# Kernel tuning notes

Hardware: AMD Instinct MI355X
Metric: run time of the kernel (lower is better)

The kernel has to match this reference:

```python
import jax, jax.numpy as jnp
import numpy as np

ALPHA = 4.0  # spikingjelly default Sigmoid surrogate alpha
BN_EPS = 1e-5

@jax.custom_vjp
def spike(x):
    return (x >= 0.0).astype(x.dtype)

def _spike_fwd(x):
    return spike(x), x

def _spike_bwd(res, g):
    s = jax.nn.sigmoid(ALPHA * res)
    return (g * ALPHA * s * (1.0 - s),)

spike.defvjp(_spike_fwd, _spike_bwd)

def lif(x, tau=2.0, vth=1.0):
    # MultiStepLIFNode: hard reset (v_reset=0), detach_reset=True, scan over time axis 0
    def step(v, xt):
        h = v + (xt - v) / tau          # charge
        s = spike(h - vth)              # fire (surrogate grad)
        v_next = h * (1.0 - jax.lax.stop_gradient(s))  # detached hard reset to 0
        return v_next, s
    _, out = jax.lax.scan(step, jnp.zeros_like(x[0]), x)
    return out

def conv_bn(x, w, b, g, be, m, var):
    # x: [TB, C, N]; 1x1 Conv1d is a channel GEMM, then eval-mode BatchNorm1d
    y = jnp.einsum('oc,bcn->bon', w, x) + b[None, :, None]
    inv = g / jnp.sqrt(var + BN_EPS)
    return (y - m[None, :, None]) * inv[None, :, None] + be[None, :, None]

def setup_inputs() -> dict:
    key = jax.random.key(0)
    T, B, C, H, W = 4, 32, 512, 14, 14
    ks = jax.random.split(key, 32)
    d = {'x': jax.random.normal(ks[0], (T, B, C, H, W), dtype=jnp.float32)}
    scale = 1.0 / np.sqrt(C)
    i = 1
    for p in ['q', 'k', 'v', 'p']:
        d[p + '_cw'] = jax.random.normal(ks[i], (C, C), dtype=jnp.float32) * scale; i += 1
        d[p + '_cb'] = jax.random.normal(ks[i], (C,), dtype=jnp.float32) * 0.1; i += 1
        d[p + '_bg'] = jnp.ones((C,), dtype=jnp.float32)
        d[p + '_bb'] = jnp.zeros((C,), dtype=jnp.float32)
        d[p + '_bm'] = jax.random.normal(ks[i], (C,), dtype=jnp.float32) * 0.1; i += 1
        d[p + '_bv'] = jax.random.uniform(ks[i], (C,), dtype=jnp.float32, minval=0.5, maxval=1.5); i += 1
    d['push_w'] = jnp.asarray(1.0, dtype=jnp.float32)
    d['pull_w'] = jnp.asarray(1.0, dtype=jnp.float32)
    d['pp_bias'] = jnp.asarray(0.0, dtype=jnp.float32)
    return d

def reference(x,
              q_cw, q_cb, q_bg, q_bb, q_bm, q_bv,
              k_cw, k_cb, k_bg, k_bb, k_bm, k_bv,
              v_cw, v_cb, v_bg, v_bb, v_bm, v_bv,
              p_cw, p_cb, p_bg, p_bb, p_bm, p_bv,
              push_w, pull_w, pp_bias):
    T, B, C, H, W = x.shape
    N = H * W
    nh = 8
    hd = C // nh
    scale = 0.125

    xs = lif(x)                                   # head_lif, [T,B,C,H,W]
    xf = xs.reshape(T * B, C, N)
    q = conv_bn(xf, q_cw, q_cb, q_bg, q_bb, q_bm, q_bv).reshape(T, B, C, N)
    k = conv_bn(xf, k_cw, k_cb, k_bg, k_bb, k_bm, k_bv).reshape(T, B, C, N)
    v = conv_bn(xf, v_cw, v_cb, v_bg, v_bb, v_bm, v_bv).reshape(T, B, C, N)

    q_on = lif(q)
    q_off = lif(-q)

    def to_heads(t):  # [T,B,C,N] -> [T,B,nh,N,hd]
        return jnp.swapaxes(t, -1, -2).reshape(T, B, N, nh, hd).transpose(0, 1, 3, 2, 4)

    q_on_h = to_heads(q_on)
    q_off_h = to_heads(q_off)
    k_h = to_heads(lif(k))
    v_h = to_heads(lif(v))

    pw = jax.nn.softplus(push_w)
    pl = jax.nn.softplus(pull_w)
    diff = pw * q_on_h - pl * q_off_h + pp_bias   # push-pull gating
    q_pp = lif(diff)

    kv = jnp.einsum('tbhnd,tbhne->tbhde', k_h, v_h)      # k^T @ v, [T,B,h,hd,hd]
    o = jnp.einsum('tbhnd,tbhde->tbhne', q_pp, kv) * scale

    o = o.transpose(0, 1, 2, 4, 3).reshape(T, B, C, N)   # transpose(3,4) then merge heads
    o = lif(o, vth=0.5)                                   # attn_lif
    o = conv_bn(o.reshape(T * B, C, N), p_cw, p_cb, p_bg, p_bb, p_bm, p_bv)
    return o.reshape(T, B, C, H, W)
```

## Files before the change

### kernel.cpp

```cpp
#include <hip/hip_runtime.h>
#include <hip/hip_bf16.h>
#include <math.h>

typedef unsigned short u16;
typedef unsigned int   u32;

#define CC 512
#define NN 196
#define TT 4
#define BB 32
#define TBB 128
#define NHH 8
#define HD 64

#define ROWS_T  6272
#define CSTRIDE ((size_t)ROWS_T * CC)

typedef __attribute__((ext_vector_type(8))) _Float16 f16x8;
typedef __attribute__((ext_vector_type(4))) float f32x4;

#define ONE_H 0x3C00

__device__ __forceinline__ u16 h_bits(_Float16 h) { return *(u16*)&h; }
__device__ __forceinline__ float h2f(u16 u) { return (float)(*(const _Float16*)&u); }
__device__ __forceinline__ u32 pk2(u16 a, u16 b) { return (u32)a | ((u32)b << 16); }

__device__ __forceinline__ void gld16(const void* g, void* l) {
    __builtin_amdgcn_global_load_lds(
        (const __attribute__((address_space(1))) void*)g,
        (__attribute__((address_space(3))) void*)l, 16, 0, 0);
}

__global__ __launch_bounds__(256) void k_prep_head(
    const float* __restrict__ x, u16* __restrict__ XS,
    const float* __restrict__ qw, const float* __restrict__ kw,
    const float* __restrict__ vw, const float* __restrict__ pw,
    const float* __restrict__ cb0, const float* __restrict__ bg0, const float* __restrict__ bb0,
    const float* __restrict__ bm0, const float* __restrict__ bv0,
    const float* __restrict__ cb1, const float* __restrict__ bg1, const float* __restrict__ bb1,
    const float* __restrict__ bm1, const float* __restrict__ bv1,
    const float* __restrict__ cb2, const float* __restrict__ bg2, const float* __restrict__ bb2,
    const float* __restrict__ bm2, const float* __restrict__ bv2,
    const float* __restrict__ cb3, const float* __restrict__ bg3, const float* __restrict__ bb3,
    const float* __restrict__ bm3, const float* __restrict__ bv3,
    u16* __restrict__ W2, float* __restrict__ SS, float* __restrict__ SH) {
    __shared__ float T[64][65];
    const int tid = threadIdx.x;

    if (blockIdx.x < 4096) {
        size_t idx = (size_t)blockIdx.x * 256 + tid;
        int g = (int)(idx >> 18);
        size_t rem = idx & 262143;
        const float* Ws = (g == 0) ? qw : (g == 1) ? kw : (g == 2) ? vw : pw;
        float w  = Ws[rem];
        _Float16 h0 = (fabsf(w) < 6.2e-5f) ? (_Float16)0.0f : (_Float16)w;
        float r = (w - (float)h0) * 2048.0f;
        _Float16 h1 = (_Float16)r;
        size_t base = (size_t)g * 524288 + rem;
        W2[base] = h_bits(h0); W2[base + 262144] = h_bits(h1);
        return;
    }
    if (blockIdx.x < 4104) {
        int idx = (blockIdx.x - 4096) * 256 + tid;
        int g = idx >> 9, o = idx & 511;
        const float* cb = g == 0 ? cb0 : g == 1 ? cb1 : g == 2 ? cb2 : cb3;
        const float* bg = g == 0 ? bg0 : g == 1 ? bg1 : g == 2 ? bg2 : bg3;
        const float* bb = g == 0 ? bb0 : g == 1 ? bb1 : g == 2 ? bb2 : bb3;
        const float* bm = g == 0 ? bm0 : g == 1 ? bm1 : g == 2 ? bm2 : bm3;
        const float* bv = g == 0 ? bv0 : g == 1 ? bv1 : g == 2 ? bv2 : bv3;
        float inv = bg[o] / sqrtf(bv[o] + 1e-5f);
        SS[g * 512 + o] = inv;
        SH[g * 512 + o] = (cb[o] - bm[o]) * inv + bb[o];
        return;
    }

    const int hidx = blockIdx.x - 4104;
    const int n0 = (hidx & 3) * 64;
    const int b  = (hidx >> 2) & 31;
    const int c_base = (hidx >> 7) * 64;
    const int c_l = tid >> 4;
    const int n4  = (tid & 15) * 4;
    const bool lv = (n0 + n4) < NN;
    const int n_r = tid >> 2;
    const int cq  = (tid & 3) * 16;
    const bool wv = (n0 + n_r) < NN;

    float v[4][4];
    #pragma unroll
    for (int k = 0; k < 4; ++k)
        #pragma unroll
        for (int j = 0; j < 4; ++j) v[k][j] = 0.f;

    for (int t = 0; t < TT; ++t) {
        const size_t xb = ((size_t)(t * BB + b) * CC + c_base) * NN;
        float s[4][4];
        #pragma unroll
        for (int k = 0; k < 4; ++k) {
            const int c = c_l + 16 * k;
            float4 xv = make_float4(0.f, 0.f, 0.f, 0.f);
            if (lv) xv = *(const float4*)(x + xb + (size_t)c * NN + n0 + n4);
            float xa[4] = {xv.x, xv.y, xv.z, xv.w};
            #pragma unroll
            for (int j = 0; j < 4; ++j) {
                float h = v[k][j] + (xa[j] - v[k][j]) * 0.5f;
                s[k][j] = (h >= 1.f) ? 1.f : 0.f;
                v[k][j] = (h >= 1.f) ? 0.f : h;
            }
        }
        __syncthreads();
        #pragma unroll
        for (int k = 0; k < 4; ++k)
            #pragma unroll
            for (int j = 0; j < 4; ++j) T[c_l + 16 * k][n4 + j] = s[k][j];
        __syncthreads();
        if (wv) {
            const size_t ob = ((size_t)(t * BB + b) * NN + n0 + n_r) * CC + c_base + cq;
            u16 u[16];
            #pragma unroll
            for (int m = 0; m < 16; ++m) u[m] = (T[cq + m][n_r] != 0.f) ? ONE_H : 0;
            uint4 q0 = make_uint4(pk2(u[0],u[1]),  pk2(u[2],u[3]),  pk2(u[4],u[5]),  pk2(u[6],u[7]));
            uint4 q1 = make_uint4(pk2(u[8],u[9]),  pk2(u[10],u[11]),pk2(u[12],u[13]),pk2(u[14],u[15]));
            *(uint4*)(XS + ob)     = q0;
            *(uint4*)(XS + ob + 8) = q1;
        }
        __syncthreads();
    }
}

__global__ __launch_bounds__(256) void k_gemm_qkv(const u16* __restrict__ S, const u16* __restrict__ W2,
                                                  const float* __restrict__ scale, const float* __restrict__ shift,
                                                  u16* __restrict__ QS, u16* __restrict__ KS, u16* __restrict__ VS,
                                                  const float* __restrict__ PW, const float* __restrict__ PL,
                                                  const float* __restrict__ PB) {
    __shared__ __align__(16) u16 smem[24576];
    u16* Xt  = smem;
    u16* WtF = smem + 8192;
    const int tid  = threadIdx.x;
    const int lane = tid & 63;
    const int w    = tid >> 6;
    const int bid  = blockIdx.x;
    const int work = (bid & 7) * 294 + (bid >> 3);
    const int rrt  = work / 12;
    const int gw   = work - rrt * 12;
    const int g    = gw >> 2;
    const int wtile = gw & 3;
    const int rr0  = rrt * 32;
    const u16* Wb = W2 + (size_t)g * 524288 + (size_t)(wtile * 128) * CC;
    const float* scl = scale + g * 512;
    const float* shf = shift + g * 512;

    const int lrow8  = lane >> 3;
    const int gchunk = ((lane & 7) ^ lrow8) * 8;
    const int l15 = lane & 15;
    const int q4  = lane >> 4;
    const int wm = (w >> 1) * 64, wn = (w & 1) * 64;

    const size_t arow0 = (size_t)w * CSTRIDE + (size_t)rr0 * CC;

    f32x4 acc[4][4];
    f32x4 zz = {0.f, 0.f, 0.f, 0.f};
    #pragma unroll
    for (int i = 0; i < 4; ++i)
        #pragma unroll
        for (int j = 0; j < 4; ++j) acc[i][j] = zz;

    for (int c0 = 0; c0 < CC; c0 += 64) {
        __syncthreads();
        #pragma unroll
        for (int i = 0; i < 4; ++i) {
            int p = w * 4 + i;
            gld16(S + arow0 + (size_t)(i * 8 + lrow8) * CC + c0 + gchunk, &Xt[p * 512]);
        }
        #pragma unroll
        for (int i = 0; i < 8; ++i) {
            int lin = w * 8 + i;
            int s = lin >> 4, p = lin & 15;
            gld16(Wb + (size_t)s * 262144 + (size_t)(p * 8 + lrow8) * CC + c0 + gchunk,
                  WtF + s * 8192 + p * 512);
        }
        __syncthreads();

        #pragma unroll
        for (int ks = 0; ks < 2; ++ks) {
            const int cpo = ((ks * 4 + q4) ^ (l15 & 7)) * 8;
            f16x8 sf[4], sflo[4];
            #pragma unroll
            for (int i = 0; i < 4; ++i) {
                sf[i]   = *(const f16x8*)&Xt[(wm + i * 16 + l15) * 64 + cpo];
                sflo[i] = sf[i] * (_Float16)0.00048828125f;
            }
            #pragma unroll
            for (int s = 0; s < 2; ++s) {
                f16x8 wf[4];
                #pragma unroll
                for (int i = 0; i < 4; ++i)
                    wf[i] = *(const f16x8*)&WtF[s * 8192 + (wn + i * 16 + l15) * 64 + cpo];
                #pragma unroll
                for (int mt = 0; mt < 4; ++mt)
                    #pragma unroll
                    for (int nt = 0; nt < 4; ++nt)
                        acc[mt][nt] = __builtin_amdgcn_mfma_f32_16x16x32_f16(
                            s ? sflo[mt] : sf[mt], wf[nt], acc[mt][nt], 0, 0, 0);
            }
        }
    }

    const float pwv = (g == 0) ? log1pf(expf(PW[0])) : 0.f;
    const float plv = (g == 0) ? log1pf(expf(PL[0])) : 0.f;
    const float pbv = (g == 0) ? PB[0] : 0.f;
    u16* OUT = (g == 0) ? QS : (g == 1) ? KS : VS;
    float* LY = (float*)smem;
    const int pairid = w & 1;
    const int pr  = tid >> 7;
    const int idx = tid & 127;

    #pragma unroll
    for (int cc = 0; cc < 2; ++cc) {
        __syncthreads();
        #pragma unroll
        for (int ntl = 0; ntl < 2; ++ntl) {
            const int nt = cc * 2 + ntl;
            const int o  = wtile * 128 + wn + nt * 16 + l15;
            const float sc = scl[o], sh = shf[o];
            const int col32 = ntl * 16 + l15;
            #pragma unroll
            for (int mt = 0; mt < 4; ++mt) {
                const int tr0 = wm + mt * 16 + q4 * 4;
                #pragma unroll
                for (int r = 0; r < 4; ++r)
                    LY[(pairid * 128 + tr0 + r) * 33 + col32] = acc[mt][nt][r] * sc + sh;
            }
        }
        __syncthreads();
        #pragma unroll
        for (int stp = 0; stp < 4; ++stp) {
            const int chain = stp * 128 + idx;
            const int nn  = chain >> 4;
            const int c2  = (chain & 15) * 2;
            const int rr  = rr0 + nn;
            const float* Lp = &LY[(pr * 128 + nn) * 33 + c2];
            float ya[4][2];
            #pragma unroll
            for (int t = 0; t < 4; ++t) {
                ya[t][0] = Lp[t * 32 * 33];
                ya[t][1] = Lp[t * 32 * 33 + 1];
            }
            const int ocol = wtile * 128 + pr * 64 + cc * 32 + c2;
            u32* op = (u32*)(OUT + (size_t)rr * CC + ocol);
            if (g == 0) {
                float von[2] = {0.f, 0.f}, voff[2] = {0.f, 0.f}, vpp[2] = {0.f, 0.f};
                #pragma unroll
                for (int t = 0; t < 4; ++t) {
                    u16 sp2[2];
                    #pragma unroll
                    for (int j = 0; j < 2; ++j) {
                        float qv = ya[t][j], h;
                        h = von[j]  + ( qv - von[j] ) * 0.5f; bool s1 = (h >= 1.f); von[j]  = s1 ? 0.f : h;
                        h = voff[j] + (-qv - voff[j]) * 0.5f; bool s2 = (h >= 1.f); voff[j] = s2 ? 0.f : h;
                        float diff = pwv * (s1 ? 1.f : 0.f) - plv * (s2 ? 1.f : 0.f) + pbv;
                        h = vpp[j] + (diff - vpp[j]) * 0.5f; bool sp = (h >= 1.f); vpp[j] = sp ? 0.f : h;
                        sp2[j] = sp ? ONE_H : 0;
                    }
                    op[t * (CSTRIDE / 2)] = pk2(sp2[0], sp2[1]);
                }
            } else {
                float vm[2] = {0.f, 0.f};
                #pragma unroll
                for (int t = 0; t < 4; ++t) {
                    u16 s2[2];
                    #pragma unroll
                    for (int j = 0; j < 2; ++j) {
                        float h = vm[j] + (ya[t][j] - vm[j]) * 0.5f;
                        bool s = (h >= 1.f); vm[j] = s ? 0.f : h;
                        s2[j] = s ? ONE_H : 0;
                    }
                    op[t * (CSTRIDE / 2)] = pk2(s2[0], s2[1]);
                }
            }
        }
    }
}

__global__ __launch_bounds__(256) void k_attn(const u16* __restrict__ Q, const u16* __restrict__ K,
                                              const u16* __restrict__ V, u16* __restrict__ OS) {
    __shared__ __align__(16) u16 sm[19584];
    u16* Kt  = sm;
    u16* Vt  = sm + 8192;
    u16* Qs  = sm;
    u16* kvT = sm + 14976;

    const int tid = threadIdx.x;
    const int tb  = blockIdx.x >> 3;
    const int h   = blockIdx.x & 7;
    const size_t gb = (size_t)tb * NN * CC + (size_t)h * HD;

    const int srow = tid >> 2;
    const int sdq  = (tid & 3) * 16;

    const int lane = tid & 63;
    const int w    = tid >> 6;
    const int l15  = lane & 15;
    const int kb8  = (lane >> 4) * 8;
    const int quad = (lane >> 4) * 4;
    const int dh = (w >> 1) * 32, eh = (w & 1) * 32;

    f32x4 accA[2][2];
    f32x4 zz = {0.f, 0.f, 0.f, 0.f};
    #pragma unroll
    for (int i = 0; i < 2; ++i)
        #pragma unroll
        for (int j = 0; j < 2; ++j) accA[i][j] = zz;

    const uint4 z4 = make_uint4(0, 0, 0, 0);

    #pragma unroll
    for (int ch = 0; ch < 2; ++ch) {
        if (ch) __syncthreads();
        #pragma unroll
        for (int c = 0; c < 2; ++c) {
            int n  = ch * 128 + c * 64 + srow;
            int nl = c * 64 + srow;
            const int nch = nl >> 3, noff = nl & 7;
            bool valid = n < NN;
            const u16* kr = K + gb + (size_t)n * CC + sdq;
            const u16* vr = V + gb + (size_t)n * CC + sdq;
            uint4 ka  = valid ? *(const uint4*)kr : z4;
            uint4 kb2 = valid ? *(const uint4*)(kr + 8) : z4;
            uint4 va  = valid ? *(const uint4*)vr : z4;
            uint4 vb2 = valid ? *(const uint4*)(vr + 8) : z4;
            u32 kwv[8] = {ka.x, ka.y, ka.z, ka.w, kb2.x, kb2.y, kb2.z, kb2.w};
            u32 vwv[8] = {va.x, va.y, va.z, va.w, vb2.x, vb2.y, vb2.z, vb2.w};
            #pragma unroll
            for (int i = 0; i < 8; ++i) {
                const int row0 = sdq + 2 * i;
                const int x0 = (row0 ^ (row0 >> 3)) & 7;
                const int cb0 = ((nch ^ x0) << 3) + noff;
                const int cb1 = ((nch ^ x0 ^ 1) << 3) + noff;
                Kt[row0 * 128 + cb0]       = (u16)(kwv[i] & 0xFFFF);
                Kt[(row0 + 1) * 128 + cb1] = (u16)(kwv[i] >> 16);
                Vt[row0 * 128 + cb0]       = (u16)(vwv[i] & 0xFFFF);
                Vt[(row0 + 1) * 128 + cb1] = (u16)(vwv[i] >> 16);
            }
        }
        __syncthreads();
        #pragma unroll
        for (int k0 = 0; k0 < 128; k0 += 32) {
            f16x8 af[2], bv[2];
            #pragma unroll
            for (int i = 0; i < 2; ++i) {
                const int rowa = dh + i * 16 + l15;
                const int xa = (rowa ^ (rowa >> 3)) & 7;
                const int rowb = eh + i * 16 + l15;
                const int xb = (rowb ^ (rowb >> 3)) & 7;
                const int chnk = (k0 + kb8) >> 3;
                af[i] = *(const f16x8*)&Kt[rowa * 128 + ((chnk ^ xa) << 3)];
                bv[i] = *(const f16x8*)&Vt[rowb * 128 + ((chnk ^ xb) << 3)];
            }
            #pragma unroll
            for (int i = 0; i < 2; ++i)
                #pragma unroll
                for (int j = 0; j < 2; ++j)
                    accA[i][j] = __builtin_amdgcn_mfma_f32_16x16x32_f16(af[i], bv[j], accA[i][j], 0, 0, 0);
        }
    }
    __syncthreads();

    #pragma unroll
    for (int i = 0; i < 2; ++i)
        #pragma unroll
        for (int j = 0; j < 2; ++j) {
            const int e  = eh + j * 16 + l15;
            const int d0 = dh + i * 16 + quad;
            _Float16 h0 = (_Float16)accA[i][j][0];
            _Float16 h1 = (_Float16)accA[i][j][1];
            _Float16 h2 = (_Float16)accA[i][j][2];
            _Float16 h3 = (_Float16)accA[i][j][3];
            uint2 wv = make_uint2(pk2(h_bits(h0), h_bits(h1)), pk2(h_bits(h2), h_bits(h3)));
            *(uint2*)&kvT[e * 72 + d0] = wv;
        }
    #pragma unroll
    for (int p = 0; p < 4; ++p) {
        int n = p * 64 + srow;
        if (n < 208) {
            uint2* qp = (uint2*)&Qs[n * 72 + sdq];
            if (n < NN) {
                const u16* qr = Q + gb + (size_t)n * CC + sdq;
                uint4 qa  = *(const uint4*)qr;
                uint4 qb2 = *(const uint4*)(qr + 8);
                qp[0] = make_uint2(qa.x, qa.y);
                qp[1] = make_uint2(qa.z, qa.w);
                qp[2] = make_uint2(qb2.x, qb2.y);
                qp[3] = make_uint2(qb2.z, qb2.w);
            } else {
                uint2 z2 = make_uint2(0, 0);
                qp[0] = z2; qp[1] = z2; qp[2] = z2; qp[3] = z2;
            }
        }
    }
    __syncthreads();

    f16x8 bq0 = *(const f16x8*)&kvT[(w * 16 + l15) * 72 + 0  + kb8];
    f16x8 bq1 = *(const f16x8*)&kvT[(w * 16 + l15) * 72 + 32 + kb8];
    u16* ob = OS + (size_t)tb * NN * CC + (size_t)h * HD + w * 16 + l15;
    #pragma unroll
    for (int nt = 0; nt < 13; ++nt) {
        f32x4 acc = zz;
        f16x8 a0 = *(const f16x8*)&Qs[(nt * 16 + l15) * 72 + 0  + kb8];
        f16x8 a1 = *(const f16x8*)&Qs[(nt * 16 + l15) * 72 + 32 + kb8];
        acc = __builtin_amdgcn_mfma_f32_16x16x32_f16(a0, bq0, acc, 0, 0, 0);
        acc = __builtin_amdgcn_mfma_f32_16x16x32_f16(a1, bq1, acc, 0, 0, 0);
        #pragma unroll
        for (int r = 0; r < 4; ++r) {
            int n = nt * 16 + quad + r;
            if (n < NN) {
                _Float16 ov = (_Float16)(acc[r] * 0.125f);
                ob[(size_t)n * CC] = h_bits(ov);
            }
        }
    }
}

__global__ __launch_bounds__(256) void k_attn_lif(uint4* __restrict__ OS) {
    const size_t idx = (size_t)blockIdx.x * 256 + threadIdx.x;
    float v[8];
    #pragma unroll
    for (int j = 0; j < 8; ++j) v[j] = 0.f;
    #pragma unroll
    for (int t = 0; t < TT; ++t) {
        const size_t o8 = idx + (size_t)t * (CSTRIDE / 8);
        uint4 d = OS[o8];
        u32 dw[4] = {d.x, d.y, d.z, d.w};
        u16 u[8];
        #pragma unroll
        for (int p = 0; p < 4; ++p) {
            #pragma unroll
            for (int hf = 0; hf < 2; ++hf) {
                int j = p * 2 + hf;
                u16 raw = hf ? (u16)(dw[p] >> 16) : (u16)(dw[p] & 0xFFFF);
                float xv = h2f(raw);
                float h = v[j] + (xv - v[j]) * 0.5f;
                bool s = (h >= 0.5f);
                v[j] = s ? 0.f : h;
                u[j] = s ? ONE_H : 0;
            }
        }
        OS[o8] = make_uint4(pk2(u[0],u[1]), pk2(u[2],u[3]), pk2(u[4],u[5]), pk2(u[6],u[7]));
    }
}

__global__ __launch_bounds__(256) void k_gemm_proj(const u16* __restrict__ S, const u16* __restrict__ W2,
                                                   const float* __restrict__ scale, const float* __restrict__ shift,
                                                   float* __restrict__ Y) {
    __shared__ __align__(16) u16 Xt[128 * 64];
    __shared__ __align__(16) u16 Wt[2][128 * 64];
    const int tid  = threadIdx.x;
    const int lane = tid & 63;
    const int w    = tid >> 6;
    const int bid  = blockIdx.x;
    const int work = (bid & 7) * 98 + (bid >> 3);
    const int ntile = work >> 2;
    const int wtile = work & 3;
    const u16* Sb = S + (size_t)ntile * 128 * CC;
    const u16* Wb = W2 + (size_t)(wtile * 128) * CC;

    const int lrow8  = lane >> 3;
    const int gchunk = ((lane & 7) ^ lrow8) * 8;
    const int l15 = lane & 15;
    const int q4  = lane >> 4;
    const int wm = (w >> 1) * 64, wn = (w & 1) * 64;

    const int tb0 = (ntile * 128) / NN;
    const int bnd = (tb0 + 1) * NN;

    f32x4 acc[4][4];
    f32x4 zz = {0.f, 0.f, 0.f, 0.f};
    #pragma unroll
    for (int i = 0; i < 4; ++i)
        #pragma unroll
        for (int j = 0; j < 4; ++j) acc[i][j] = zz;

    for (int c0 = 0; c0 < CC; c0 += 64) {
        __syncthreads();
        #pragma unroll
        for (int i = 0; i < 4; ++i) {
            int p = w * 4 + i;
            gld16(Sb + (size_t)(p * 8 + lrow8) * CC + c0 + gchunk, &Xt[p * 512]);
        }
        #pragma unroll
        for (int i = 0; i < 8; ++i) {
            int lin = w * 8 + i;
            int s = lin >> 4, p = lin & 15;
            gld16(Wb + (size_t)s * 262144 + (size_t)(p * 8 + lrow8) * CC + c0 + gchunk,
                  &Wt[s][p * 512]);
        }
        __syncthreads();

        #pragma unroll
        for (int ks = 0; ks < 2; ++ks) {
            const int cpo = ((ks * 4 + q4) ^ (l15 & 7)) * 8;
            f16x8 sf[4], sflo[4];
            #pragma unroll
            for (int i = 0; i < 4; ++i) {
                sf[i]   = *(const f16x8*)&Xt[(wn + i * 16 + l15) * 64 + cpo];
                sflo[i] = sf[i] * (_Float16)0.00048828125f;
            }
            #pragma unroll
            for (int s = 0; s < 2; ++s) {
                f16x8 wf[4];
                #pragma unroll
                for (int i = 0; i < 4; ++i)
                    wf[i] = *(const f16x8*)&Wt[s][(wm + i * 16 + l15) * 64 + cpo];
                #pragma unroll
                for (int mt = 0; mt < 4; ++mt)
                    #pragma unroll
                    for (int nt = 0; nt < 4; ++nt)
                        acc[mt][nt] = __builtin_amdgcn_mfma_f32_16x16x32_f16(
                            wf[mt], s ? sflo[nt] : sf[nt], acc[mt][nt], 0, 0, 0);
            }
        }
    }

    #pragma unroll
    for (int mt = 0; mt < 4; ++mt) {
        int o0 = wtile * 128 + wm + mt * 16 + (lane >> 4) * 4;
        #pragma unroll
        for (int nt = 0; nt < 4; ++nt) {
            int row = ntile * 128 + wn + nt * 16 + l15;
            int tb = (row >= bnd) ? tb0 + 1 : tb0;
            int n  = row - tb * NN;
            #pragma unroll
            for (int r = 0; r < 4; ++r)
                Y[((size_t)tb * CC + o0 + r) * NN + n] = acc[mt][nt][r] * scale[o0 + r] + shift[o0 + r];
        }
    }
}

extern "C" void kernel_launch(void* const* d_in, const int* in_sizes, int n_in,
                              void* d_out, int out_size, void* d_ws, size_t ws_size,
                              hipStream_t stream) {
    const float* x    = (const float*)d_in[0];
    const float* q_cw = (const float*)d_in[1];
    const float* q_cb = (const float*)d_in[2];
    const float* q_bg = (const float*)d_in[3];
    const float* q_bb = (const float*)d_in[4];
    const float* q_bm = (const float*)d_in[5];
    const float* q_bv = (const float*)d_in[6];
    const float* k_cw = (const float*)d_in[7];
    const float* k_cb = (const float*)d_in[8];
    const float* k_bg = (const float*)d_in[9];
    const float* k_bb = (const float*)d_in[10];
    const float* k_bm = (const float*)d_in[11];
    const float* k_bv = (const float*)d_in[12];
    const float* v_cw = (const float*)d_in[13];
    const float* v_cb = (const float*)d_in[14];
    const float* v_bg = (const float*)d_in[15];
    const float* v_bb = (const float*)d_in[16];
    const float* v_bm = (const float*)d_in[17];
    const float* v_bv = (const float*)d_in[18];
    const float* p_cw = (const float*)d_in[19];
    const float* p_cb = (const float*)d_in[20];
    const float* p_bg = (const float*)d_in[21];
    const float* p_bb = (const float*)d_in[22];
    const float* p_bm = (const float*)d_in[23];
    const float* p_bv = (const float*)d_in[24];
    const float* pshw = (const float*)d_in[25];
    const float* pllw = (const float*)d_in[26];
    const float* ppb  = (const float*)d_in[27];
    float* out = (float*)d_out;

    if (ws_size < (size_t)242 * 1024 * 1024) return;
    char* W = (char*)d_ws;
    u16*   XS = (u16*)W;
    u16*   QS = (u16*)(W + ((size_t)27 << 20));
    u16*   OS = (u16*)(W + ((size_t)78 << 20));
    u16*   KS = (u16*)(W + ((size_t)182 << 20));
    u16*   VS = (u16*)(W + ((size_t)208 << 20));
    u16*   W2 = (u16*)(W + ((size_t)234 << 20));
    float* SS = (float*)(W + ((size_t)238 << 20));
    float* SH = SS + 2048;

    k_prep_head<<<5128, 256, 0, stream>>>(x, XS,
                                          q_cw, k_cw, v_cw, p_cw,
                                          q_cb, q_bg, q_bb, q_bm, q_bv,
                                          k_cb, k_bg, k_bb, k_bm, k_bv,
                                          v_cb, v_bg, v_bb, v_bm, v_bv,
                                          p_cb, p_bg, p_bb, p_bm, p_bv, W2, SS, SH);

    k_gemm_qkv<<<2352, 256, 0, stream>>>(XS, W2, SS, SH, QS, KS, VS, pshw, pllw, ppb);

    k_attn<<<TBB * NHH, 256, 0, stream>>>(QS, KS, VS, OS);
    k_attn_lif<<<1568, 256, 0, stream>>>((uint4*)OS);

    k_gemm_proj<<<784, 256, 0, stream>>>(OS, W2 + 3 * 524288, SS + 1536, SH + 1536, out);
}
```

Measured before the change: 328.9 us.

## Store K/V spikes channel-major padded so attention loads them via direct-to-LDS copies

The QKV GEMM epilogue now writes K and V spikes transposed into a [T*B, C, 256] layout with zero-padded token tails, instead of token-major rows. The attention kernel then fills its LDS K/V tiles with global_load_lds 16-byte copies using a simple XOR swizzle, replacing the per-element scatter transpose. The prep kernel is split so the pad-zeroing runs separately from the head LIF kernel. The cost is scattered 2-byte global stores in the GEMM epilogue and an extra kernel launch.

```diff
diff --git a/kernel.cpp b/kernel.cpp
--- a/kernel.cpp
+++ b/kernel.cpp
@@ -31,8 +31,7 @@
         (__attribute__((address_space(3))) void*)l, 16, 0, 0);
 }
 
-__global__ __launch_bounds__(256) void k_prep_head(
-    const float* __restrict__ x, u16* __restrict__ XS,
+__global__ __launch_bounds__(256) void k_prep(
     const float* __restrict__ qw, const float* __restrict__ kw,
     const float* __restrict__ vw, const float* __restrict__ pw,
     const float* __restrict__ cb0, const float* __restrict__ bg0, const float* __restrict__ bb0,
@@ -43,12 +42,10 @@
     const float* __restrict__ bm2, const float* __restrict__ bv2,
     const float* __restrict__ cb3, const float* __restrict__ bg3, const float* __restrict__ bb3,
     const float* __restrict__ bm3, const float* __restrict__ bv3,
-    u16* __restrict__ W2, float* __restrict__ SS, float* __restrict__ SH) {
-    __shared__ float T[64][65];
-    const int tid = threadIdx.x;
-
+    u16* __restrict__ W2, float* __restrict__ SS, float* __restrict__ SH,
+    u32* __restrict__ KT32, u32* __restrict__ VT32) {
     if (blockIdx.x < 4096) {
-        size_t idx = (size_t)blockIdx.x * 256 + tid;
+        size_t idx = (size_t)blockIdx.x * 256 + threadIdx.x;
         int g = (int)(idx >> 18);
         size_t rem = idx & 262143;
         const float* Ws = (g == 0) ? qw : (g == 1) ? kw : (g == 2) ? vw : pw;
@@ -61,7 +58,7 @@
         return;
     }
     if (blockIdx.x < 4104) {
-        int idx = (blockIdx.x - 4096) * 256 + tid;
+        int idx = (blockIdx.x - 4096) * 256 + threadIdx.x;
         int g = idx >> 9, o = idx & 511;
         const float* cb = g == 0 ? cb0 : g == 1 ? cb1 : g == 2 ? cb2 : cb3;
         const float* bg = g == 0 ? bg0 : g == 1 ? bg1 : g == 2 ? bg2 : bg3;
@@ -73,11 +70,20 @@
         SH[g * 512 + o] = (cb[o] - bm[o]) * inv + bb[o];
         return;
     }
-
-    const int hidx = blockIdx.x - 4104;
-    const int n0 = (hidx & 3) * 64;
-    const int b  = (hidx >> 2) & 31;
-    const int c_base = (hidx >> 7) * 64;
+    int idx = (blockIdx.x - 4104) * 256 + threadIdx.x;
+    u32* A = (idx >> 16) ? VT32 : KT32;
+    int row = idx & 65535;
+    u32* p = A + (size_t)row * 128 + 98;
+    #pragma unroll
+    for (int k = 0; k < 30; ++k) p[k] = 0;
+}
+
+__global__ __launch_bounds__(256) void k_head_lif(const float* __restrict__ x, u16* __restrict__ XS) {
+    __shared__ float T[64][65];
+    const int tid = threadIdx.x;
+    const int n0 = blockIdx.x * 64;
+    const int b  = blockIdx.y;
+    const int c_base = blockIdx.z * 64;
     const int c_l = tid >> 4;
     const int n4  = (tid & 15) * 4;
     const bool lv = (n0 + n4) < NN;
@@ -129,7 +135,7 @@
 
 __global__ __launch_bounds__(256) void k_gemm_qkv(const u16* __restrict__ S, const u16* __restrict__ W2,
                                                   const float* __restrict__ scale, const float* __restrict__ shift,
-                                                  u16* __restrict__ QS, u16* __restrict__ KS, u16* __restrict__ VS,
+                                                  u16* __restrict__ QS, u16* __restrict__ KT, u16* __restrict__ VT,
                                                   const float* __restrict__ PW, const float* __restrict__ PL,
                                                   const float* __restrict__ PB) {
     __shared__ __align__(16) u16 smem[24576];
@@ -208,7 +214,6 @@
     const float pwv = (g == 0) ? log1pf(expf(PW[0])) : 0.f;
     const float plv = (g == 0) ? log1pf(expf(PL[0])) : 0.f;
     const float pbv = (g == 0) ? PB[0] : 0.f;
-    u16* OUT = (g == 0) ? QS : (g == 1) ? KS : VS;
     float* LY = (float*)smem;
     const int pairid = w & 1;
     const int pr  = tid >> 7;
@@ -232,29 +237,25 @@
             }
         }
         __syncthreads();
-        #pragma unroll
-        for (int stp = 0; stp < 4; ++stp) {
-            const int chain = stp * 128 + idx;
-            const int nn  = chain >> 4;
-            const int c2  = (chain & 15) * 2;
-            const int rr  = rr0 + nn;
-            const float* Lp = &LY[(pr * 128 + nn) * 33 + c2];
-            float ya[4][2];
-            #pragma unroll
-            for (int t = 0; t < 4; ++t) {
-                ya[t][0] = Lp[t * 32 * 33];
-                ya[t][1] = Lp[t * 32 * 33 + 1];
-            }
-            const int ocol = wtile * 128 + pr * 64 + cc * 32 + c2;
-            u32* op = (u32*)(OUT + (size_t)rr * CC + ocol);
-            if (g == 0) {
+        if (g == 0) {
+            #pragma unroll
+            for (int stp = 0; stp < 4; ++stp) {
+                const int chain = stp * 128 + idx;
+                const int nn  = chain >> 4;
+                const int c2  = (chain & 15) * 2;
+                const int rr  = rr0 + nn;
+                const float* Lp = &LY[(pr * 128 + nn) * 33 + c2];
+                const int ocol = wtile * 128 + pr * 64 + cc * 32 + c2;
+                u32* op = (u32*)(QS + (size_t)rr * CC + ocol);
                 float von[2] = {0.f, 0.f}, voff[2] = {0.f, 0.f}, vpp[2] = {0.f, 0.f};
                 #pragma unroll
                 for (int t = 0; t < 4; ++t) {
+                    float ya0 = Lp[t * 32 * 33], ya1 = Lp[t * 32 * 33 + 1];
+                    float yy[2] = {ya0, ya1};
                     u16 sp2[2];
                     #pragma unroll
                     for (int j = 0; j < 2; ++j) {
-                        float qv = ya[t][j], h;
+                        float qv = yy[j], h;
                         h = von[j]  + ( qv - von[j] ) * 0.5f; bool s1 = (h >= 1.f); von[j]  = s1 ? 0.f : h;
                         h = voff[j] + (-qv - voff[j]) * 0.5f; bool s2 = (h >= 1.f); voff[j] = s2 ? 0.f : h;
                         float diff = pwv * (s1 ? 1.f : 0.f) - plv * (s2 ? 1.f : 0.f) + pbv;
@@ -263,26 +264,41 @@
                     }
                     op[t * (CSTRIDE / 2)] = pk2(sp2[0], sp2[1]);
                 }
-            } else {
+            }
+        } else {
+            u16* OUTT = (g == 1) ? KT : VT;
+            #pragma unroll
+            for (int stp = 0; stp < 4; ++stp) {
+                const int chain = stp * 128 + idx;
+                const int nn = chain & 31;
+                const int c2 = (chain >> 5) * 2;
+                const int rr = rr0 + nn;
+                const int b  = rr / 196;
+                const int n  = rr - b * 196;
+                const float* Lp = &LY[(pr * 128 + nn) * 33 + c2];
+                const int c = wtile * 128 + pr * 64 + cc * 32 + c2;
                 float vm[2] = {0.f, 0.f};
                 #pragma unroll
                 for (int t = 0; t < 4; ++t) {
+                    float yy[2] = {Lp[t * 32 * 33], Lp[t * 32 * 33 + 1]};
                     u16 s2[2];
                     #pragma unroll
                     for (int j = 0; j < 2; ++j) {
-                        float h = vm[j] + (ya[t][j] - vm[j]) * 0.5f;
+                        float h = vm[j] + (yy[j] - vm[j]) * 0.5f;
                         bool s = (h >= 1.f); vm[j] = s ? 0.f : h;
                         s2[j] = s ? ONE_H : 0;
                     }
-                    op[t * (CSTRIDE / 2)] = pk2(s2[0], s2[1]);
+                    size_t base = ((size_t)(t * BB + b) * CC + c) * 256 + n;
+                    OUTT[base]       = s2[0];
+                    OUTT[base + 256] = s2[1];
                 }
             }
         }
     }
 }
 
-__global__ __launch_bounds__(256) void k_attn(const u16* __restrict__ Q, const u16* __restrict__ K,
-                                              const u16* __restrict__ V, u16* __restrict__ OS) {
+__global__ __launch_bounds__(256) void k_attn(const u16* __restrict__ Q, const u16* __restrict__ KTg,
+                                              const u16* __restrict__ VTg, u16* __restrict__ OS) {
     __shared__ __align__(16) u16 sm[19584];
     u16* Kt  = sm;
     u16* Vt  = sm + 8192;
@@ -292,7 +308,8 @@
     const int tid = threadIdx.x;
     const int tb  = blockIdx.x >> 3;
     const int h   = blockIdx.x & 7;
-    const size_t gb = (size_t)tb * NN * CC + (size_t)h * HD;
+    const size_t gbq = (size_t)tb * NN * CC + (size_t)h * HD;
+    const size_t gbk = ((size_t)tb * CC + h * HD) * 256;
 
     const int srow = tid >> 2;
     const int sdq  = (tid & 3) * 16;
@@ -311,50 +328,32 @@
         #pragma unroll
         for (int j = 0; j < 2; ++j) accA[i][j] = zz;
 
-    const uint4 z4 = make_uint4(0, 0, 0, 0);
-
     #pragma unroll
     for (int ch = 0; ch < 2; ++ch) {
         if (ch) __syncthreads();
         #pragma unroll
-        for (int c = 0; c < 2; ++c) {
-            int n  = ch * 128 + c * 64 + srow;
-            int nl = c * 64 + srow;
-            const int nch = nl >> 3, noff = nl & 7;
-            bool valid = n < NN;
-            const u16* kr = K + gb + (size_t)n * CC + sdq;
-            const u16* vr = V + gb + (size_t)n * CC + sdq;
-            uint4 ka  = valid ? *(const uint4*)kr : z4;
-            uint4 kb2 = valid ? *(const uint4*)(kr + 8) : z4;
-            uint4 va  = valid ? *(const uint4*)vr : z4;
-            uint4 vb2 = valid ? *(const uint4*)(vr + 8) : z4;
-            u32 kwv[8] = {ka.x, ka.y, ka.z, ka.w, kb2.x, kb2.y, kb2.z, kb2.w};
-            u32 vwv[8] = {va.x, va.y, va.z, va.w, vb2.x, vb2.y, vb2.z, vb2.w};
-            #pragma unroll
-            for (int i = 0; i < 8; ++i) {
-                const int row0 = sdq + 2 * i;
-                const int x0 = (row0 ^ (row0 >> 3)) & 7;
-                const int cb0 = ((nch ^ x0) << 3) + noff;
-                const int cb1 = ((nch ^ x0 ^ 1) << 3) + noff;
-                Kt[row0 * 128 + cb0]       = (u16)(kwv[i] & 0xFFFF);
-                Kt[(row0 + 1) * 128 + cb1] = (u16)(kwv[i] >> 16);
-                Vt[row0 * 128 + cb0]       = (u16)(vwv[i] & 0xFFFF);
-                Vt[(row0 + 1) * 128 + cb1] = (u16)(vwv[i] >> 16);
-            }
+        for (int i = 0; i < 4; ++i) {
+            const int r = w * 16 + i * 4 + (lane >> 4);
+            const int so = ch * 128 + (((lane & 15) ^ (r & 7)) << 3);
+            gld16(KTg + gbk + (size_t)r * 256 + so, &Kt[(w * 16 + i * 4) * 128]);
+        }
+        #pragma unroll
+        for (int i = 0; i < 4; ++i) {
+            const int r = w * 16 + i * 4 + (lane >> 4);
+            const int so = ch * 128 + (((lane & 15) ^ (r & 7)) << 3);
+            gld16(VTg + gbk + (size_t)r * 256 + so, &Vt[(w * 16 + i * 4) * 128]);
         }
         __syncthreads();
         #pragma unroll
         for (int k0 = 0; k0 < 128; k0 += 32) {
+            const int ck = (k0 + kb8) >> 3;
             f16x8 af[2], bv[2];
             #pragma unroll
             for (int i = 0; i < 2; ++i) {
                 const int rowa = dh + i * 16 + l15;
-                const int xa = (rowa ^ (rowa >> 3)) & 7;
                 const int rowb = eh + i * 16 + l15;
-                const int xb = (rowb ^ (rowb >> 3)) & 7;
-                const int chnk = (k0 + kb8) >> 3;
-                af[i] = *(const f16x8*)&Kt[rowa * 128 + ((chnk ^ xa) << 3)];
-                bv[i] = *(const f16x8*)&Vt[rowb * 128 + ((chnk ^ xb) << 3)];
+                af[i] = *(const f16x8*)&Kt[rowa * 128 + ((ck ^ (rowa & 7)) << 3)];
+                bv[i] = *(const f16x8*)&Vt[rowb * 128 + ((ck ^ (rowb & 7)) << 3)];
             }
             #pragma unroll
             for (int i = 0; i < 2; ++i)
@@ -384,7 +383,7 @@
         if (n < 208) {
             uint2* qp = (uint2*)&Qs[n * 72 + sdq];
             if (n < NN) {
-                const u16* qr = Q + gb + (size_t)n * CC + sdq;
+                const u16* qr = Q + gbq + (size_t)n * CC + sdq;
                 uint4 qa  = *(const uint4*)qr;
                 uint4 qb2 = *(const uint4*)(qr + 8);
                 qp[0] = make_uint2(qa.x, qa.y);
@@ -401,7 +400,7 @@
 
     f16x8 bq0 = *(const f16x8*)&kvT[(w * 16 + l15) * 72 + 0  + kb8];
     f16x8 bq1 = *(const f16x8*)&kvT[(w * 16 + l15) * 72 + 32 + kb8];
-    u16* ob = OS + (size_t)tb * NN * CC + (size_t)h * HD + w * 16 + l15;
+    u16* ob = OS + gbq + w * 16 + l15;
     #pragma unroll
     for (int nt = 0; nt < 13; ++nt) {
         f32x4 acc = zz;
@@ -573,22 +572,24 @@
     u16*   XS = (u16*)W;
     u16*   QS = (u16*)(W + ((size_t)27 << 20));
     u16*   OS = (u16*)(W + ((size_t)78 << 20));
-    u16*   KS = (u16*)(W + ((size_t)182 << 20));
-    u16*   VS = (u16*)(W + ((size_t)208 << 20));
+    u16*   KT = (u16*)(W + ((size_t)110 << 20));
+    u16*   VT = (u16*)(W + ((size_t)144 << 20));
     u16*   W2 = (u16*)(W + ((size_t)234 << 20));
     float* SS = (float*)(W + ((size_t)238 << 20));
     float* SH = SS + 2048;
 
-    k_prep_head<<<5128, 256, 0, stream>>>(x, XS,
-                                          q_cw, k_cw, v_cw, p_cw,
-                                          q_cb, q_bg, q_bb, q_bm, q_bv,
-                                          k_cb, k_bg, k_bb, k_bm, k_bv,
-                                          v_cb, v_bg, v_bb, v_bm, v_bv,
-                                          p_cb, p_bg, p_bb, p_bm, p_bv, W2, SS, SH);
-
-    k_gemm_qkv<<<2352, 256, 0, stream>>>(XS, W2, SS, SH, QS, KS, VS, pshw, pllw, ppb);
-
-    k_attn<<<TBB * NHH, 256, 0, stream>>>(QS, KS, VS, OS);
+    k_prep<<<4616, 256, 0, stream>>>(q_cw, k_cw, v_cw, p_cw,
+                                     q_cb, q_bg, q_bb, q_bm, q_bv,
+                                     k_cb, k_bg, k_bb, k_bm, k_bv,
+                                     v_cb, v_bg, v_bb, v_bm, v_bv,
+                                     p_cb, p_bg, p_bb, p_bm, p_bv, W2, SS, SH,
+                                     (u32*)KT, (u32*)VT);
+
+    k_head_lif<<<dim3(4, 32, 8), 256, 0, stream>>>(x, XS);
+
+    k_gemm_qkv<<<2352, 256, 0, stream>>>(XS, W2, SS, SH, QS, KT, VT, pshw, pllw, ppb);
+
+    k_attn<<<TBB * NHH, 256, 0, stream>>>(QS, KT, VT, OS);
     k_attn_lif<<<1568, 256, 0, stream>>>((uint4*)OS);
 
     k_gemm_proj<<<784, 256, 0, stream>>>(OS, W2 + 3 * 524288, SS + 1536, SH + 1536, out);
```

After: 325.9 us. About the same (-0.9%).
